# Kernel optimization log

Measured on AMD Instinct MI355X. Metric: run time of the kernel, lower is better.

## Reference

```python
import jax, jax.numpy as jnp
import numpy as np

NEG_INF = -9e15


def setup_inputs() -> dict:
    key = jax.random.key(0)
    k1, k2, k3, k4 = jax.random.split(key, 4)
    N, F_in, H, F_out = 4096, 512, 8, 64
    node_features = jax.random.normal(k1, (N, F_in), dtype=jnp.float32)
    adj_matrix = jax.random.randint(k2, (N, N), 0, 2, dtype=jnp.int32)
    # ensure self-loops so every row has at least one unmasked entry
    adj_matrix = jnp.maximum(adj_matrix, jnp.eye(N, dtype=jnp.int32))
    W = jax.random.normal(k3, (H, F_in, F_out), dtype=jnp.float32) * 0.05
    a = jax.random.normal(k4, (H, 2 * F_out), dtype=jnp.float32) * 0.05
    return {"node_features": node_features, "adj_matrix": adj_matrix, "W": W, "a": a}


def reference(node_features, adj_matrix, W, a):
    alpha = 0.2
    H, F_in, F_out = W.shape
    # Per-head linear projection: [H, N, F_out]
    Wh = jnp.einsum("nf,hfo->hno", node_features, W)
    # Attention logits e_ij = LeakyReLU(a1 . Wh_i + a2 . Wh_j)
    f_src = jnp.einsum("hno,ho->hn", Wh, a[:, :F_out])   # [H, N]
    f_dst = jnp.einsum("hno,ho->hn", Wh, a[:, F_out:])   # [H, N]
    e = jax.nn.leaky_relu(f_src[:, :, None] + f_dst[:, None, :], negative_slope=alpha)  # [H, N, N]
    # Mask by adjacency, softmax over neighbors
    masked = jnp.where(adj_matrix[None, :, :] > 0, e, NEG_INF)
    attn = jax.nn.softmax(masked, axis=-1)               # [H, N, N]
    # Aggregate neighbor features per head
    h_prime = jnp.einsum("hnm,hmo->hno", attn, Wh)       # [H, N, F_out]
    # Concat heads along feature dim -> [N, H*F_out]
    return jnp.transpose(h_prime, (1, 0, 2)).reshape(h_prime.shape[1], H * F_out)
```

## Files before the change

kernel.cpp:

```cpp
#include <hip/hip_runtime.h>
#include <hip/hip_bf16.h>
#include <stdint.h>


#define NN 4096
#define FIN 512
#define NH 8
#define FO 64

typedef __attribute__((ext_vector_type(8))) short bf16x8;
typedef __attribute__((ext_vector_type(4))) float f32x4;

#define GLOAD_LDS16(g, l)                                                          \
  __builtin_amdgcn_global_load_lds((__attribute__((address_space(1))) const void*)(g), \
                                   (__attribute__((address_space(3))) void*)(l), 16, 0, 0)
#define GLOAD_LDS4(g, l)                                                           \
  __builtin_amdgcn_global_load_lds((__attribute__((address_space(1))) const void*)(g), \
                                   (__attribute__((address_space(3))) void*)(l), 4, 0, 0)

__device__ __forceinline__ unsigned short f2bf(float f) {
  unsigned u = __float_as_uint(f);
  u += 0x7fffu + ((u >> 16) & 1u);
  return (unsigned short)(u >> 16);
}

__global__ __launch_bounds__(256) void prep_kernel(
    const float* __restrict__ X, const int* __restrict__ adj, const float* __restrict__ W,
    const float* __restrict__ a,
    unsigned short* __restrict__ Xb, unsigned short* __restrict__ WbT,
    unsigned* __restrict__ adjbitsT, unsigned short* __restrict__ WAb) {
  int bid = blockIdx.x, tid = threadIdx.x;
  if (bid < 2048) {
    int item = bid * 256 + tid;
    int jt = item >> 12, r = item & 4095;
    const int* p = adj + (size_t)r * NN + jt * 32;
    unsigned bits = 0;
#pragma unroll
    for (int b = 0; b < 32; b += 4) {
      int4 v = *(const int4*)(p + b);
      bits |= (unsigned)(v.x & 1) << b;
      bits |= (unsigned)(v.y & 1) << (b + 1);
      bits |= (unsigned)(v.z & 1) << (b + 2);
      bits |= (unsigned)(v.w & 1) << (b + 3);
    }
    adjbitsT[item] = bits;
  } else if (bid < 4096) {
    int item = (bid - 2048) * 256 + tid;
    float4 v = ((const float4*)X)[item];
    ushort4 o;
    o.x = f2bf(v.x); o.y = f2bf(v.y); o.z = f2bf(v.z); o.w = f2bf(v.w);
    ((ushort4*)Xb)[item] = o;
  } else if (bid < 5120) {
    int item = (bid - 4096) * 256 + tid;
    int h = item >> 15, rem = item & 32767, o = rem >> 9, k = rem & 511;
    WbT[item] = f2bf(W[h * (FIN * FO) + k * FO + o]);
  } else {
    int item = (bid - 5120) * 256 + tid;
    int h = item >> 10, which = (item >> 9) & 1, k = item & 511;
    const float4* wp = (const float4*)(W + ((size_t)h * FIN + k) * FO);
    const float4* ap = (const float4*)(a + h * 128 + which * 64);
    float s = 0.f;
#pragma unroll
    for (int o4 = 0; o4 < 16; ++o4) {
      float4 w4 = wp[o4], a4 = ap[o4];
      s += w4.x * a4.x + w4.y * a4.y + w4.z * a4.z + w4.w * a4.w;
    }
    WAb[(h * 2 + which) * FIN + k] = f2bf(s);
  }
}

__global__ __launch_bounds__(256, 4) void proj_sd_kernel(
    const unsigned short* __restrict__ Xb, const unsigned short* __restrict__ WbT,
    const unsigned short* __restrict__ WAb,
    unsigned short* __restrict__ Whfrag, float2* __restrict__ ABf,
    float2* __restrict__ E12f) {
  int lane = threadIdx.x & 63, wave = threadIdx.x >> 6;
  int row16 = lane & 15, grp = lane >> 4;
  if (blockIdx.y == 8) {
    int i0 = (blockIdx.x * 4 + wave) * 16;
    f32x4 acc = {0, 0, 0, 0};
    const unsigned short* xb = Xb + (size_t)(i0 + row16) * FIN + grp * 8;
    const unsigned short* wb = WAb + row16 * FIN + grp * 8;
#pragma unroll
    for (int k0 = 0; k0 < FIN; k0 += 32)
      acc = __builtin_amdgcn_mfma_f32_16x16x32_bf16(*(const bf16x8*)(xb + k0),
                                                    *(const bf16x8*)(wb + k0), acc, 0, 0, 0);
    int hh = row16 >> 1;
#pragma unroll
    for (int reg = 0; reg < 4; ++reg) {
      int rr = i0 + grp * 4 + reg;
      float v = acc[reg];
      if (row16 & 1) {
        E12f[hh * NN + rr] = make_float2(__expf(v), __expf(0.2f * v));
      } else {
        ABf[hh * NN + rr] = make_float2(__expf(v), __expf(0.2f * v));
      }
    }
    return;
  }
  int h = blockIdx.y;
  int i0 = blockIdx.x * 64 + wave * 16;
  f32x4 acc[4] = {{0,0,0,0},{0,0,0,0},{0,0,0,0},{0,0,0,0}};
  const unsigned short* xb = Xb + (size_t)(i0 + row16) * FIN + grp * 8;
  const unsigned short* wb = WbT + h * (FO * FIN) + row16 * FIN + grp * 8;
#pragma unroll 4
  for (int k0 = 0; k0 < FIN; k0 += 32) {
    bf16x8 af = *(const bf16x8*)(xb + k0);
#pragma unroll
    for (int cb = 0; cb < 4; ++cb)
      acc[cb] = __builtin_amdgcn_mfma_f32_16x16x32_bf16(
          af, *(const bf16x8*)(wb + cb * 16 * FIN + k0), acc[cb], 0, 0, 0);
  }
  int jt = i0 >> 5;
  int kk0 = (i0 & 31) + grp * 4;
  int tl = (kk0 >> 3) * 16 + row16;
  int e0 = kk0 & 7;
#pragma unroll
  for (int cb = 0; cb < 4; ++cb) {
    ushort4 pk;
    pk.x = f2bf(acc[cb][0]); pk.y = f2bf(acc[cb][1]);
    pk.z = f2bf(acc[cb][2]); pk.w = f2bf(acc[cb][3]);
    *(ushort4*)(Whfrag + (((size_t)h * 128 + jt) * 4 + cb) * 512 + tl * 8 + e0) = pk;
  }
}

#define SEGB 18432
#define E_OFF 16384
#define A_OFF 17408
#define PH 4
#define NPHASE 16

__global__ __launch_bounds__(512, 4) void gat_kernel(
    const unsigned* __restrict__ adjbitsT, const unsigned short* __restrict__ Whfrag,
    const float2* __restrict__ ABf, const float2* __restrict__ E12f,
    float* __restrict__ out) {
  __shared__ char lds[4 * SEGB];
  int h = blockIdx.y;
  int lane = threadIdx.x & 63, wave = threadIdx.x >> 6;
  int row16 = lane & 15, grp = lane >> 4;
  int rt = wave >> 1, jseg = wave & 1;
  int r0 = blockIdx.x * 64;
  int i0 = r0 + rt * 16;
  int r = i0 + row16;
  float2 ab = ABf[h * NN + r];
  float Ai = ab.x, Bi = ab.y;

  bf16x8 ones;
#pragma unroll
  for (int e = 0; e < 8; ++e) ones[e] = (short)0x3F80;

  const unsigned short* wsrc = Whfrag + (size_t)h * 262144 + lane * 8;
  const float2* esrc = E12f + h * NN + lane * 2;

  f32x4 a0 = {0,0,0,0}, a1 = {0,0,0,0}, a2 = {0,0,0,0}, ad = {0,0,0,0}, aden = {0,0,0,0};

  auto stage = [&](int buf, int p) {
    int jt = jseg * 64 + p * PH + rt;
    char* base = lds + (jseg * 2 + buf) * SEGB;
    const unsigned short* bs = wsrc + (size_t)jt * 2048;
    char* bd = base + rt * 4096;
    GLOAD_LDS16(bs, bd);
    GLOAD_LDS16(bs + 512, bd + 1024);
    GLOAD_LDS16(bs + 1024, bd + 2048);
    GLOAD_LDS16(bs + 1536, bd + 3072);
    GLOAD_LDS4(adjbitsT + (size_t)jt * NN + r0 + lane, base + A_OFF + rt * 256);
    if (rt == 0)
      GLOAD_LDS16(esrc + (size_t)(jseg * 64 + p * PH) * 32, base + E_OFF);
  };

  auto compute = [&](int buf) {
    char* base = lds + (jseg * 2 + buf) * SEGB;
#pragma unroll
    for (int t = 0; t < PH; ++t) {
      unsigned bw = *(const unsigned*)(base + A_OFF + t * 256 + (rt * 16 + row16) * 4);
      unsigned bb = (bw >> (grp * 8)) & 0xffu;
      const f32x4* ep = (const f32x4*)(base + E_OFF + t * 256 + grp * 64);
      f32x4 ev0 = ep[0], ev1 = ep[1], ev2 = ep[2], ev3 = ep[3];
      const char* bbase = base + t * 4096 + lane * 16;
      bf16x8 b0 = *(const bf16x8*)(bbase);
      bf16x8 b1 = *(const bf16x8*)(bbase + 1024);
      bf16x8 b2 = *(const bf16x8*)(bbase + 2048);
      bf16x8 b3 = *(const bf16x8*)(bbase + 3072);
      float v[8];
      v[0] = fmaxf(Ai * ev0[0], Bi * ev0[1]);
      v[1] = fmaxf(Ai * ev0[2], Bi * ev0[3]);
      v[2] = fmaxf(Ai * ev1[0], Bi * ev1[1]);
      v[3] = fmaxf(Ai * ev1[2], Bi * ev1[3]);
      v[4] = fmaxf(Ai * ev2[0], Bi * ev2[1]);
      v[5] = fmaxf(Ai * ev2[2], Bi * ev2[3]);
      v[6] = fmaxf(Ai * ev3[0], Bi * ev3[1]);
      v[7] = fmaxf(Ai * ev3[2], Bi * ev3[3]);
      bf16x8 af;
#pragma unroll
      for (int e = 0; e < 8; ++e) {
        float val = (bb & (1u << e)) ? v[e] : 0.0f;
        __hip_bfloat16 hb = __float2bfloat16(val);
        af[e] = *reinterpret_cast<short*>(&hb);
      }
      a0   = __builtin_amdgcn_mfma_f32_16x16x32_bf16(af, b0, a0, 0, 0, 0);
      a1   = __builtin_amdgcn_mfma_f32_16x16x32_bf16(af, b1, a1, 0, 0, 0);
      a2   = __builtin_amdgcn_mfma_f32_16x16x32_bf16(af, b2, a2, 0, 0, 0);
      aden = __builtin_amdgcn_mfma_f32_16x16x32_bf16(af, ones, aden, 0, 0, 0);
      ad   = __builtin_amdgcn_mfma_f32_16x16x32_bf16(af, b3, ad, 0, 0, 0);
    }
  };

  stage(0, 0);
  __syncthreads();
  int b = 0;
#pragma unroll 1
  for (int p = 0; p < NPHASE; ++p) {
    if (p < NPHASE - 1) stage(b ^ 1, p + 1);
    compute(b);
    __syncthreads();
    b ^= 1;
  }

  float* red = (float*)lds;
  if (jseg == 1) {
    float* q = red + (rt * 64 + lane) * 20;
    *(f32x4*)(q +  0) = a0;
    *(f32x4*)(q +  4) = a1;
    *(f32x4*)(q +  8) = a2;
    *(f32x4*)(q + 12) = ad;
    *(f32x4*)(q + 16) = aden;
  }
  __syncthreads();
  if (jseg == 0) {
    const float* q = red + (rt * 64 + lane) * 20;
    a0   += *(const f32x4*)(q +  0);
    a1   += *(const f32x4*)(q +  4);
    a2   += *(const f32x4*)(q +  8);
    ad   += *(const f32x4*)(q + 12);
    aden += *(const f32x4*)(q + 16);
#pragma unroll
    for (int reg = 0; reg < 4; ++reg) {
      float inv = 1.0f / aden[reg];
      int row = i0 + grp * 4 + reg;
      float* op = out + (size_t)row * (NH * FO) + h * FO + row16;
      op[0]  = a0[reg] * inv;
      op[16] = a1[reg] * inv;
      op[32] = a2[reg] * inv;
      op[48] = ad[reg] * inv;
    }
  }
}

extern "C" void kernel_launch(void* const* d_in, const int* in_sizes, int n_in,
                              void* d_out, int out_size, void* d_ws, size_t ws_size,
                              hipStream_t stream) {
  const float* X  = (const float*)d_in[0];
  const int* adj  = (const int*)d_in[1];
  const float* W  = (const float*)d_in[2];
  const float* a  = (const float*)d_in[3];
  float* out = (float*)d_out;
  char* ws = (char*)d_ws;

  unsigned short* Xb     = (unsigned short*)(ws + 0);
  unsigned short* WbT    = (unsigned short*)(ws + 4194304);
  unsigned* adjbitsT     = (unsigned*)(ws + 4718592);
  unsigned short* Whfrag = (unsigned short*)(ws + 6815744);
  unsigned short* WAb    = (unsigned short*)(ws + 11010048);
  float2* ABf            = (float2*)(ws + 11026432);
  float2* E12f           = (float2*)(ws + 11288576);

  prep_kernel<<<5152, 256, 0, stream>>>(X, adj, W, a, Xb, WbT, adjbitsT, WAb);
  proj_sd_kernel<<<dim3(64, 9), 256, 0, stream>>>(Xb, WbT, WAb, Whfrag, ABf, E12f);
  gat_kernel<<<dim3(64, 8), 512, 0, stream>>>(adjbitsT, Whfrag, ABf, E12f, out);
}
```

Measured before the change: 89.12 us.

## Switch GAT pipeline to fp16 with packed attention math and smaller LDS stages

Converts all intermediate operands from bf16 to fp16 and uses the f16 MFMA. The attention weights are now built with packed half2 multiply/max, and the adjacency mask is applied by multiplying with 0/1 half values. The exp factors are stored as separate fp16 arrays, and A/B are prescaled by 0.5 to avoid fp16 overflow. The per-stage LDS tile is halved (2 tiles per phase, 32 phases) so more blocks can stay resident, and staging loads are split across waves. These changes cut the scalar conversion and mask ALU work in the inner loop. The risks are fp16 range and precision issues in the exp products, plus doubled synchronisation count.

```diff
diff --git a/kernel.cpp b/kernel.cpp
--- a/kernel.cpp
+++ b/kernel.cpp
@@ -1,5 +1,4 @@
 #include <hip/hip_runtime.h>
-#include <hip/hip_bf16.h>
 #include <stdint.h>
 
 
@@ -8,8 +7,12 @@
 #define NH 8
 #define FO 64
 
-typedef __attribute__((ext_vector_type(8))) short bf16x8;
+typedef _Float16 f16x8 __attribute__((ext_vector_type(8)));
+typedef _Float16 f16x2 __attribute__((ext_vector_type(2)));
 typedef __attribute__((ext_vector_type(4))) float f32x4;
+
+union H8 { f16x8 v; f16x2 p[4]; unsigned u[4]; };
+union U2 { unsigned u; f16x2 v; };
 
 #define GLOAD_LDS16(g, l)                                                          \
   __builtin_amdgcn_global_load_lds((__attribute__((address_space(1))) const void*)(g), \
@@ -18,17 +21,16 @@
   __builtin_amdgcn_global_load_lds((__attribute__((address_space(1))) const void*)(g), \
                                    (__attribute__((address_space(3))) void*)(l), 4, 0, 0)
 
-__device__ __forceinline__ unsigned short f2bf(float f) {
-  unsigned u = __float_as_uint(f);
-  u += 0x7fffu + ((u >> 16) & 1u);
-  return (unsigned short)(u >> 16);
+__device__ __forceinline__ unsigned short f2h(float f) {
+  _Float16 h = (_Float16)f;
+  return __builtin_bit_cast(unsigned short, h);
 }
 
 __global__ __launch_bounds__(256) void prep_kernel(
     const float* __restrict__ X, const int* __restrict__ adj, const float* __restrict__ W,
     const float* __restrict__ a,
-    unsigned short* __restrict__ Xb, unsigned short* __restrict__ WbT,
-    unsigned* __restrict__ adjbitsT, unsigned short* __restrict__ WAb) {
+    unsigned short* __restrict__ Xh, unsigned short* __restrict__ WbT,
+    unsigned* __restrict__ adjbitsT, unsigned short* __restrict__ WAh) {
   int bid = blockIdx.x, tid = threadIdx.x;
   if (bid < 2048) {
     int item = bid * 256 + tid;
@@ -48,12 +50,12 @@
     int item = (bid - 2048) * 256 + tid;
     float4 v = ((const float4*)X)[item];
     ushort4 o;
-    o.x = f2bf(v.x); o.y = f2bf(v.y); o.z = f2bf(v.z); o.w = f2bf(v.w);
-    ((ushort4*)Xb)[item] = o;
+    o.x = f2h(v.x); o.y = f2h(v.y); o.z = f2h(v.z); o.w = f2h(v.w);
+    ((ushort4*)Xh)[item] = o;
   } else if (bid < 5120) {
     int item = (bid - 4096) * 256 + tid;
     int h = item >> 15, rem = item & 32767, o = rem >> 9, k = rem & 511;
-    WbT[item] = f2bf(W[h * (FIN * FO) + k * FO + o]);
+    WbT[item] = f2h(W[h * (FIN * FO) + k * FO + o]);
   } else {
     int item = (bid - 5120) * 256 + tid;
     int h = item >> 10, which = (item >> 9) & 1, k = item & 511;
@@ -65,33 +67,34 @@
       float4 w4 = wp[o4], a4 = ap[o4];
       s += w4.x * a4.x + w4.y * a4.y + w4.z * a4.z + w4.w * a4.w;
     }
-    WAb[(h * 2 + which) * FIN + k] = f2bf(s);
+    WAh[(h * 2 + which) * FIN + k] = f2h(s);
   }
 }
 
 __global__ __launch_bounds__(256, 4) void proj_sd_kernel(
-    const unsigned short* __restrict__ Xb, const unsigned short* __restrict__ WbT,
-    const unsigned short* __restrict__ WAb,
+    const unsigned short* __restrict__ Xh, const unsigned short* __restrict__ WbT,
+    const unsigned short* __restrict__ WAh,
     unsigned short* __restrict__ Whfrag, float2* __restrict__ ABf,
-    float2* __restrict__ E12f) {
+    unsigned short* __restrict__ E1h, unsigned short* __restrict__ E2h) {
   int lane = threadIdx.x & 63, wave = threadIdx.x >> 6;
   int row16 = lane & 15, grp = lane >> 4;
   if (blockIdx.y == 8) {
     int i0 = (blockIdx.x * 4 + wave) * 16;
     f32x4 acc = {0, 0, 0, 0};
-    const unsigned short* xb = Xb + (size_t)(i0 + row16) * FIN + grp * 8;
-    const unsigned short* wb = WAb + row16 * FIN + grp * 8;
+    const unsigned short* xb = Xh + (size_t)(i0 + row16) * FIN + grp * 8;
+    const unsigned short* wb = WAh + row16 * FIN + grp * 8;
 #pragma unroll
     for (int k0 = 0; k0 < FIN; k0 += 32)
-      acc = __builtin_amdgcn_mfma_f32_16x16x32_bf16(*(const bf16x8*)(xb + k0),
-                                                    *(const bf16x8*)(wb + k0), acc, 0, 0, 0);
+      acc = __builtin_amdgcn_mfma_f32_16x16x32_f16(*(const f16x8*)(xb + k0),
+                                                   *(const f16x8*)(wb + k0), acc, 0, 0, 0);
     int hh = row16 >> 1;
 #pragma unroll
     for (int reg = 0; reg < 4; ++reg) {
       int rr = i0 + grp * 4 + reg;
       float v = acc[reg];
       if (row16 & 1) {
-        E12f[hh * NN + rr] = make_float2(__expf(v), __expf(0.2f * v));
+        E1h[hh * NN + rr] = f2h(__expf(v));
+        E2h[hh * NN + rr] = f2h(__expf(0.2f * v));
       } else {
         ABf[hh * NN + rr] = make_float2(__expf(v), __expf(0.2f * v));
       }
@@ -101,15 +104,15 @@
   int h = blockIdx.y;
   int i0 = blockIdx.x * 64 + wave * 16;
   f32x4 acc[4] = {{0,0,0,0},{0,0,0,0},{0,0,0,0},{0,0,0,0}};
-  const unsigned short* xb = Xb + (size_t)(i0 + row16) * FIN + grp * 8;
+  const unsigned short* xb = Xh + (size_t)(i0 + row16) * FIN + grp * 8;
   const unsigned short* wb = WbT + h * (FO * FIN) + row16 * FIN + grp * 8;
 #pragma unroll 4
   for (int k0 = 0; k0 < FIN; k0 += 32) {
-    bf16x8 af = *(const bf16x8*)(xb + k0);
+    f16x8 af = *(const f16x8*)(xb + k0);
 #pragma unroll
     for (int cb = 0; cb < 4; ++cb)
-      acc[cb] = __builtin_amdgcn_mfma_f32_16x16x32_bf16(
-          af, *(const bf16x8*)(wb + cb * 16 * FIN + k0), acc[cb], 0, 0, 0);
+      acc[cb] = __builtin_amdgcn_mfma_f32_16x16x32_f16(
+          af, *(const f16x8*)(wb + cb * 16 * FIN + k0), acc[cb], 0, 0, 0);
   }
   int jt = i0 >> 5;
   int kk0 = (i0 & 31) + grp * 4;
@@ -118,23 +121,23 @@
 #pragma unroll
   for (int cb = 0; cb < 4; ++cb) {
     ushort4 pk;
-    pk.x = f2bf(acc[cb][0]); pk.y = f2bf(acc[cb][1]);
-    pk.z = f2bf(acc[cb][2]); pk.w = f2bf(acc[cb][3]);
+    pk.x = f2h(acc[cb][0]); pk.y = f2h(acc[cb][1]);
+    pk.z = f2h(acc[cb][2]); pk.w = f2h(acc[cb][3]);
     *(ushort4*)(Whfrag + (((size_t)h * 128 + jt) * 4 + cb) * 512 + tl * 8 + e0) = pk;
   }
 }
 
-#define SEGB 18432
-#define E_OFF 16384
-#define A_OFF 17408
-#define PH 4
-#define NPHASE 16
-
-__global__ __launch_bounds__(512, 4) void gat_kernel(
+#define SEGB 9216
+#define E_OFF 8192
+#define A_OFF 8448
+#define PH 2
+#define NPHASE 32
+
+__global__ __launch_bounds__(512, 8) void gat_kernel(
     const unsigned* __restrict__ adjbitsT, const unsigned short* __restrict__ Whfrag,
-    const float2* __restrict__ ABf, const float2* __restrict__ E12f,
-    float* __restrict__ out) {
-  __shared__ char lds[4 * SEGB];
+    const float2* __restrict__ ABf, const unsigned short* __restrict__ E1h,
+    const unsigned short* __restrict__ E2h, float* __restrict__ out) {
+  __shared__ __align__(16) char lds[4 * SEGB];
   int h = blockIdx.y;
   int lane = threadIdx.x & 63, wave = threadIdx.x >> 6;
   int row16 = lane & 15, grp = lane >> 4;
@@ -143,29 +146,38 @@
   int i0 = r0 + rt * 16;
   int r = i0 + row16;
   float2 ab = ABf[h * NN + r];
-  float Ai = ab.x, Bi = ab.y;
-
-  bf16x8 ones;
-#pragma unroll
-  for (int e = 0; e < 8; ++e) ones[e] = (short)0x3F80;
+  _Float16 Ah1 = (_Float16)(0.5f * ab.x);
+  _Float16 Bh1 = (_Float16)(0.5f * ab.y);
+  f16x2 Ah = {Ah1, Ah1}, Bh = {Bh1, Bh1};
+
+  H8 ones;
+#pragma unroll
+  for (int k = 0; k < 4; ++k) ones.u[k] = 0x3C003C00u;
 
   const unsigned short* wsrc = Whfrag + (size_t)h * 262144 + lane * 8;
-  const float2* esrc = E12f + h * NN + lane * 2;
+  const unsigned short* e1src = E1h + h * NN + jseg * 2048 + lane * 8;
+  const unsigned short* e2src = E2h + h * NN + jseg * 2048 + lane * 8;
 
   f32x4 a0 = {0,0,0,0}, a1 = {0,0,0,0}, a2 = {0,0,0,0}, ad = {0,0,0,0}, aden = {0,0,0,0};
 
   auto stage = [&](int buf, int p) {
-    int jt = jseg * 64 + p * PH + rt;
     char* base = lds + (jseg * 2 + buf) * SEGB;
-    const unsigned short* bs = wsrc + (size_t)jt * 2048;
-    char* bd = base + rt * 4096;
-    GLOAD_LDS16(bs, bd);
-    GLOAD_LDS16(bs + 512, bd + 1024);
-    GLOAD_LDS16(bs + 1024, bd + 2048);
-    GLOAD_LDS16(bs + 1536, bd + 3072);
-    GLOAD_LDS4(adjbitsT + (size_t)jt * NN + r0 + lane, base + A_OFF + rt * 256);
-    if (rt == 0)
-      GLOAD_LDS16(esrc + (size_t)(jseg * 64 + p * PH) * 32, base + E_OFF);
+    int jt0 = jseg * 64 + p * PH;
+    if (rt < 2) {
+      const unsigned short* bs = wsrc + (size_t)(jt0 + rt) * 2048;
+      char* bd = base + rt * 4096;
+      GLOAD_LDS16(bs, bd);
+      GLOAD_LDS16(bs + 512, bd + 1024);
+      GLOAD_LDS16(bs + 1024, bd + 2048);
+      GLOAD_LDS16(bs + 1536, bd + 3072);
+    } else {
+      int t = rt - 2;
+      GLOAD_LDS4(adjbitsT + (size_t)(jt0 + t) * NN + r0 + lane, base + A_OFF + t * 256);
+      if (lane < 8) {
+        const unsigned short* es = (t == 0 ? e1src : e2src) + p * (PH * 32);
+        GLOAD_LDS16(es, base + E_OFF + t * 128);
+      }
+    }
   };
 
   auto compute = [&](int buf) {
@@ -174,34 +186,27 @@
     for (int t = 0; t < PH; ++t) {
       unsigned bw = *(const unsigned*)(base + A_OFF + t * 256 + (rt * 16 + row16) * 4);
       unsigned bb = (bw >> (grp * 8)) & 0xffu;
-      const f32x4* ep = (const f32x4*)(base + E_OFF + t * 256 + grp * 64);
-      f32x4 ev0 = ep[0], ev1 = ep[1], ev2 = ep[2], ev3 = ep[3];
+      H8 e1, e2;
+      e1.v = *(const f16x8*)(base + E_OFF + t * 64 + grp * 16);
+      e2.v = *(const f16x8*)(base + E_OFF + 128 + t * 64 + grp * 16);
       const char* bbase = base + t * 4096 + lane * 16;
-      bf16x8 b0 = *(const bf16x8*)(bbase);
-      bf16x8 b1 = *(const bf16x8*)(bbase + 1024);
-      bf16x8 b2 = *(const bf16x8*)(bbase + 2048);
-      bf16x8 b3 = *(const bf16x8*)(bbase + 3072);
-      float v[8];
-      v[0] = fmaxf(Ai * ev0[0], Bi * ev0[1]);
-      v[1] = fmaxf(Ai * ev0[2], Bi * ev0[3]);
-      v[2] = fmaxf(Ai * ev1[0], Bi * ev1[1]);
-      v[3] = fmaxf(Ai * ev1[2], Bi * ev1[3]);
-      v[4] = fmaxf(Ai * ev2[0], Bi * ev2[1]);
-      v[5] = fmaxf(Ai * ev2[2], Bi * ev2[3]);
-      v[6] = fmaxf(Ai * ev3[0], Bi * ev3[1]);
-      v[7] = fmaxf(Ai * ev3[2], Bi * ev3[3]);
-      bf16x8 af;
-#pragma unroll
-      for (int e = 0; e < 8; ++e) {
-        float val = (bb & (1u << e)) ? v[e] : 0.0f;
-        __hip_bfloat16 hb = __float2bfloat16(val);
-        af[e] = *reinterpret_cast<short*>(&hb);
+      f16x8 b0 = *(const f16x8*)(bbase);
+      f16x8 b1 = *(const f16x8*)(bbase + 1024);
+      f16x8 b2 = *(const f16x8*)(bbase + 2048);
+      f16x8 b3 = *(const f16x8*)(bbase + 3072);
+      H8 af;
+#pragma unroll
+      for (int k = 0; k < 4; ++k) {
+        f16x2 mx = __builtin_elementwise_max(Ah * e1.p[k], Bh * e2.p[k]);
+        U2 m;
+        m.u = (((bb >> (2 * k)) & 1u) << 14) | (((bb >> (2 * k + 1)) & 1u) << 30);
+        af.p[k] = mx * m.v;
       }
-      a0   = __builtin_amdgcn_mfma_f32_16x16x32_bf16(af, b0, a0, 0, 0, 0);
-      a1   = __builtin_amdgcn_mfma_f32_16x16x32_bf16(af, b1, a1, 0, 0, 0);
-      a2   = __builtin_amdgcn_mfma_f32_16x16x32_bf16(af, b2, a2, 0, 0, 0);
-      aden = __builtin_amdgcn_mfma_f32_16x16x32_bf16(af, ones, aden, 0, 0, 0);
-      ad   = __builtin_amdgcn_mfma_f32_16x16x32_bf16(af, b3, ad, 0, 0, 0);
+      a0   = __builtin_amdgcn_mfma_f32_16x16x32_f16(af.v, b0, a0, 0, 0, 0);
+      a1   = __builtin_amdgcn_mfma_f32_16x16x32_f16(af.v, b1, a1, 0, 0, 0);
+      a2   = __builtin_amdgcn_mfma_f32_16x16x32_f16(af.v, b2, a2, 0, 0, 0);
+      aden = __builtin_amdgcn_mfma_f32_16x16x32_f16(af.v, ones.v, aden, 0, 0, 0);
+      ad   = __builtin_amdgcn_mfma_f32_16x16x32_f16(af.v, b3, ad, 0, 0, 0);
     }
   };
 
@@ -256,15 +261,16 @@
   float* out = (float*)d_out;
   char* ws = (char*)d_ws;
 
-  unsigned short* Xb     = (unsigned short*)(ws + 0);
+  unsigned short* Xh     = (unsigned short*)(ws + 0);
   unsigned short* WbT    = (unsigned short*)(ws + 4194304);
   unsigned* adjbitsT     = (unsigned*)(ws + 4718592);
   unsigned short* Whfrag = (unsigned short*)(ws + 6815744);
-  unsigned short* WAb    = (unsigned short*)(ws + 11010048);
+  unsigned short* WAh    = (unsigned short*)(ws + 11010048);
   float2* ABf            = (float2*)(ws + 11026432);
-  float2* E12f           = (float2*)(ws + 11288576);
-
-  prep_kernel<<<5152, 256, 0, stream>>>(X, adj, W, a, Xb, WbT, adjbitsT, WAb);
-  proj_sd_kernel<<<dim3(64, 9), 256, 0, stream>>>(Xb, WbT, WAb, Whfrag, ABf, E12f);
-  gat_kernel<<<dim3(64, 8), 512, 0, stream>>>(adjbitsT, Whfrag, ABf, E12f, out);
-}
+  unsigned short* E1h    = (unsigned short*)(ws + 11288576);
+  unsigned short* E2h    = (unsigned short*)(ws + 11354112);
+
+  prep_kernel<<<5152, 256, 0, stream>>>(X, adj, W, a, Xh, WbT, adjbitsT, WAh);
+  proj_sd_kernel<<<dim3(64, 9), 256, 0, stream>>>(Xh, WbT, WAh, Whfrag, ABf, E1h, E2h);
+  gat_kernel<<<dim3(64, 8), 512, 0, stream>>>(adjbitsT, Whfrag, ABf, E1h, E2h, out);
+}
```

Result: faster. 82.03 us (-8.0%).
